# Optimization experiments

Hardware: AMD Instinct MI355X
Metric: run time of the kernel (lower is better)

The kernel has to match this reference:

```python
import jax, jax.numpy as jnp
import numpy as np

UP = 2      # up_ratio
K = 3       # kernel_size
EPS = 1e-5  # BatchNorm eps


def _bn(x, g, b, m, v):
    # eval-mode BatchNorm2d over channel axis 1 of NCHW
    scale = g / jnp.sqrt(v + EPS)
    return x * scale[:, None, None] + (b - m * scale)[:, None, None]


def setup_inputs() -> dict:
    key = jax.random.key(0)
    ks = jax.random.split(key, 13)
    N, C, H, W = 8, 256, 64, 64
    OC = 64
    P = UP * UP * K * K  # 36 encoder output channels
    return {
        "x": jax.random.normal(ks[0], (N, C, H, W), jnp.float32),
        "w0": jax.random.normal(ks[1], (OC, C), jnp.float32) * 0.05,
        "b0": jax.random.normal(ks[2], (OC,), jnp.float32) * 0.05,
        "bn0_g": jax.random.uniform(ks[3], (OC,), jnp.float32, 0.5, 1.5),
        "bn0_b": jax.random.normal(ks[4], (OC,), jnp.float32) * 0.05,
        "bn0_m": jax.random.normal(ks[5], (OC,), jnp.float32) * 0.05,
        "bn0_v": jax.random.uniform(ks[6], (OC,), jnp.float32, 0.5, 1.5),
        "w1": jax.random.normal(ks[7], (P, OC), jnp.float32) * 0.05,
        "b1": jax.random.normal(ks[8], (P,), jnp.float32) * 0.05,
        "bn1_g": jax.random.uniform(ks[9], (P,), jnp.float32, 0.5, 1.5),
        "bn1_b": jax.random.normal(ks[10], (P,), jnp.float32) * 0.05,
        "bn1_m": jax.random.normal(ks[11], (P,), jnp.float32) * 0.05,
        "bn1_v": jax.random.uniform(ks[12], (P,), jnp.float32, 0.5, 1.5),
    }


def reference(x, w0, b0, bn0_g, bn0_b, bn0_m, bn0_v,
              w1, b1, bn1_g, bn1_b, bn1_m, bn1_v):
    N, C, H, W = x.shape
    k2, u2 = K * K, UP * UP

    # layer0: 1x1 conv + BN + ReLU
    y = jnp.einsum('nchw,oc->nohw', x, w0) + b0[:, None, None]
    y = jax.nn.relu(_bn(y, bn0_g, bn0_b, bn0_m, bn0_v))

    # encoder: 1x1 conv + BN + ReLU -> (N, u2*k2, H, W)
    enc = jnp.einsum('nohw,po->nphw', y, w1) + b1[:, None, None]
    enc = jax.nn.relu(_bn(enc, bn1_g, bn1_b, bn1_m, bn1_v))

    # pixelshuffle(UP) + softmax over k2 + unfold back to low-res is
    # algebraically: split channels as (k2, u2) and softmax over k2.
    # channel index = k*u2 + r*UP + s, matching torch PixelShuffle layout.
    wts = jax.nn.softmax(enc.reshape(N, k2, u2, H, W), axis=1)  # n k u h w

    # im2col on input: ZeroPad2d(1) + 3x3 unfold -> (N, C, k2, H, W)
    pad = K // 2
    xp = jnp.pad(x, ((0, 0), (0, 0), (pad, pad), (pad, pad)))
    patches = jnp.stack([xp[:, :, i:i + H, j:j + W]
                         for i in range(K) for j in range(K)], axis=2)

    out = jnp.einsum('nckhw,nkuhw->ncuhw', patches, wts)  # (N, C, u2, H, W)

    # pixelshuffle: u = r*UP + s places value at (h*UP+r, w*UP+s)
    out = out.reshape(N, C, UP, UP, H, W)
    out = out.transpose(0, 1, 4, 2, 5, 3).reshape(N, C, H * UP, W * UP)
    return out
```

## Files before the change

kernel.cpp:

```cpp
#include <hip/hip_runtime.h>


#define EPS_BN 1e-5f

typedef float f32x4 __attribute__((ext_vector_type(4)));

__global__ __launch_bounds__(256) void carafe_fused(
    const float* __restrict__ x,
    const float* __restrict__ w0, const float* __restrict__ b0,
    const float* __restrict__ g0, const float* __restrict__ be0,
    const float* __restrict__ m0, const float* __restrict__ v0,
    const float* __restrict__ w1, const float* __restrict__ b1,
    const float* __restrict__ g1, const float* __restrict__ be1,
    const float* __restrict__ m1, const float* __restrict__ v1,
    float* __restrict__ out)
{
    __shared__ float xs[256 * 64];
    __shared__ float ys[64 * 64];

    const int tid = threadIdx.x;
    const int n   = blockIdx.x >> 6;
    const int hh  = blockIdx.x & 63;
    const int w   = tid & 63;
    const int og  = __builtin_amdgcn_readfirstlane(tid >> 6);

    {
        const f32x4* xg = reinterpret_cast<const f32x4*>(x + (n * 256) * 4096 + hh * 64);
        f32x4* xl = reinterpret_cast<f32x4*>(xs);
#pragma unroll
        for (int k = 0; k < 16; ++k) {
            const int i  = tid + k * 256;
            const int cc = i >> 4;
            const int c4 = i & 15;
            xl[cc * 16 + c4] = xg[cc * 1024 + c4];
        }
    }
    __syncthreads();

    float acc[16];
#pragma unroll
    for (int j = 0; j < 16; ++j) acc[j] = 0.f;

    const float* w0p = w0 + og * 16 * 256;
#pragma unroll 8
    for (int c = 0; c < 256; ++c) {
        const float xv = xs[c * 64 + w];
#pragma unroll
        for (int j = 0; j < 16; ++j)
            acc[j] = fmaf(xv, w0p[j * 256 + c], acc[j]);
    }

#pragma unroll
    for (int j = 0; j < 16; ++j) {
        const int o = og * 16 + j;
        const float sc = g0[o] * rsqrtf(v0[o] + EPS_BN);
        const float sh = (b0[o] - m0[o]) * sc + be0[o];
        ys[o * 64 + w] = fmaxf(fmaf(acc[j], sc, sh), 0.f);
    }
    __syncthreads();

    float e9[9];
#pragma unroll
    for (int kk = 0; kk < 9; ++kk) e9[kk] = 0.f;
    const int u = og;
    const float* w1p = w1 + u * 64;
#pragma unroll 4
    for (int o = 0; o < 64; ++o) {
        const float yv = ys[o * 64 + w];
#pragma unroll
        for (int kk = 0; kk < 9; ++kk)
            e9[kk] = fmaf(yv, w1p[kk * 256 + o], e9[kk]);
    }

    float mx = -1e30f;
#pragma unroll
    for (int kk = 0; kk < 9; ++kk) {
        const int p = kk * 4 + u;
        const float sc = g1[p] * rsqrtf(v1[p] + EPS_BN);
        const float sh = (b1[p] - m1[p]) * sc + be1[p];
        float e = fmaxf(fmaf(e9[kk], sc, sh), 0.f);
        e9[kk] = e;
        mx = fmaxf(mx, e);
    }
    float s = 0.f;
#pragma unroll
    for (int kk = 0; kk < 9; ++kk) {
        e9[kk] = __expf(e9[kk] - mx);
        s += e9[kk];
    }
    const float inv = 1.f / s;

    __syncthreads();
    float* ws = ys;
#pragma unroll
    for (int kk = 0; kk < 9; ++kk)
        ws[(kk * 4 + u) * 64 + w] = e9[kk] * inv;
    __syncthreads();

    const int q = og;
    float wt[36];
#pragma unroll
    for (int p = 0; p < 36; ++p) wt[p] = ws[p * 64 + w];

    const bool hm = (hh > 0), hp = (hh < 63);
    const bool wm = (w > 0),  wp = (w < 63);

    for (int c = 0; c < 64; ++c) {
        const int cc = q * 64 + c;
        const float* xgm = x + ((n * 256 + cc) * 64 + (hh - 1)) * 64;
        const float* xgp = x + ((n * 256 + cc) * 64 + (hh + 1)) * 64;
        const float* xls = xs + cc * 64;

        float a0 = 0.f, a1 = 0.f, a2 = 0.f, a3 = 0.f;

        {
            const float xv0 = (hm & wm) ? xgm[w - 1] : 0.f;
            const float xv1 = hm        ? xgm[w]     : 0.f;
            const float xv2 = (hm & wp) ? xgm[w + 1] : 0.f;
            a0 = fmaf(xv0, wt[0],  fmaf(xv1, wt[4],  xv2 * wt[8]));
            a1 = fmaf(xv0, wt[1],  fmaf(xv1, wt[5],  xv2 * wt[9]));
            a2 = fmaf(xv0, wt[2],  fmaf(xv1, wt[6],  xv2 * wt[10]));
            a3 = fmaf(xv0, wt[3],  fmaf(xv1, wt[7],  xv2 * wt[11]));
        }
        {
            const float xv0 = wm ? xls[w - 1] : 0.f;
            const float xv1 = xls[w];
            const float xv2 = wp ? xls[w + 1] : 0.f;
            a0 = fmaf(xv0, wt[12], fmaf(xv1, wt[16], fmaf(xv2, wt[20], a0)));
            a1 = fmaf(xv0, wt[13], fmaf(xv1, wt[17], fmaf(xv2, wt[21], a1)));
            a2 = fmaf(xv0, wt[14], fmaf(xv1, wt[18], fmaf(xv2, wt[22], a2)));
            a3 = fmaf(xv0, wt[15], fmaf(xv1, wt[19], fmaf(xv2, wt[23], a3)));
        }
        {
            const float xv0 = (hp & wm) ? xgp[w - 1] : 0.f;
            const float xv1 = hp        ? xgp[w]     : 0.f;
            const float xv2 = (hp & wp) ? xgp[w + 1] : 0.f;
            a0 = fmaf(xv0, wt[24], fmaf(xv1, wt[28], fmaf(xv2, wt[32], a0)));
            a1 = fmaf(xv0, wt[25], fmaf(xv1, wt[29], fmaf(xv2, wt[33], a1)));
            a2 = fmaf(xv0, wt[26], fmaf(xv1, wt[30], fmaf(xv2, wt[34], a2)));
            a3 = fmaf(xv0, wt[27], fmaf(xv1, wt[31], fmaf(xv2, wt[35], a3)));
        }

        float* op = out + ((n * 256 + cc) * 128 + 2 * hh) * 128 + 2 * w;
        float2 r0; r0.x = a0; r0.y = a1;
        float2 r1; r1.x = a2; r1.y = a3;
        *reinterpret_cast<float2*>(op)       = r0;
        *reinterpret_cast<float2*>(op + 128) = r1;
    }
}

extern "C" void kernel_launch(void* const* d_in, const int* in_sizes, int n_in,
                              void* d_out, int out_size, void* d_ws, size_t ws_size,
                              hipStream_t stream)
{
    const float* x   = (const float*)d_in[0];
    const float* w0  = (const float*)d_in[1];
    const float* b0  = (const float*)d_in[2];
    const float* g0  = (const float*)d_in[3];
    const float* be0 = (const float*)d_in[4];
    const float* m0  = (const float*)d_in[5];
    const float* v0  = (const float*)d_in[6];
    const float* w1  = (const float*)d_in[7];
    const float* b1  = (const float*)d_in[8];
    const float* g1  = (const float*)d_in[9];
    const float* be1 = (const float*)d_in[10];
    const float* m1  = (const float*)d_in[11];
    const float* v1  = (const float*)d_in[12];

    float* out = (float*)d_out;

    hipLaunchKernelGGL(carafe_fused, dim3(512), dim3(256), 0, stream,
                       x, w0, b0, g0, be0, m0, v0, w1, b1, g1, be1, m1, v1, out);
}
```

Baseline: 244.7 us.

## Drop 64KB input LDS stage and double block to 512 threads

```diff
diff --git a/kernel.cpp b/kernel.cpp
--- a/kernel.cpp
+++ b/kernel.cpp
@@ -3,9 +3,7 @@
 
 #define EPS_BN 1e-5f
 
-typedef float f32x4 __attribute__((ext_vector_type(4)));
-
-__global__ __launch_bounds__(256) void carafe_fused(
+__global__ __launch_bounds__(512, 4) void carafe_fused(
     const float* __restrict__ x,
     const float* __restrict__ w0, const float* __restrict__ b0,
     const float* __restrict__ g0, const float* __restrict__ be0,
@@ -15,7 +13,6 @@
     const float* __restrict__ m1, const float* __restrict__ v1,
     float* __restrict__ out)
 {
-    __shared__ float xs[256 * 64];
     __shared__ float ys[64 * 64];
 
     const int tid = threadIdx.x;
@@ -24,35 +21,24 @@
     const int w   = tid & 63;
     const int og  = __builtin_amdgcn_readfirstlane(tid >> 6);
 
-    {
-        const f32x4* xg = reinterpret_cast<const f32x4*>(x + (n * 256) * 4096 + hh * 64);
-        f32x4* xl = reinterpret_cast<f32x4*>(xs);
+    float acc[8];
 #pragma unroll
-        for (int k = 0; k < 16; ++k) {
-            const int i  = tid + k * 256;
-            const int cc = i >> 4;
-            const int c4 = i & 15;
-            xl[cc * 16 + c4] = xg[cc * 1024 + c4];
-        }
-    }
-    __syncthreads();
+    for (int j = 0; j < 8; ++j) acc[j] = 0.f;
 
-    float acc[16];
-#pragma unroll
-    for (int j = 0; j < 16; ++j) acc[j] = 0.f;
+    const float* xp  = x + n * 1048576 + hh * 64 + w;
+    const float* w0p = w0 + og * 8 * 256;
 
-    const float* w0p = w0 + og * 16 * 256;
 #pragma unroll 8
     for (int c = 0; c < 256; ++c) {
-        const float xv = xs[c * 64 + w];
+        const float xv = xp[c * 4096];
 #pragma unroll
-        for (int j = 0; j < 16; ++j)
+        for (int j = 0; j < 8; ++j)
             acc[j] = fmaf(xv, w0p[j * 256 + c], acc[j]);
     }
 
 #pragma unroll
-    for (int j = 0; j < 16; ++j) {
-        const int o = og * 16 + j;
+    for (int j = 0; j < 8; ++j) {
+        const int o = og * 8 + j;
         const float sc = g0[o] * rsqrtf(v0[o] + EPS_BN);
         const float sh = (b0[o] - m0[o]) * sc + be0[o];
         ys[o * 64 + w] = fmaxf(fmaf(acc[j], sc, sh), 0.f);
@@ -62,9 +48,9 @@
     float e9[9];
 #pragma unroll
     for (int kk = 0; kk < 9; ++kk) e9[kk] = 0.f;
-    const int u = og;
+    const int u = og & 3;
     const float* w1p = w1 + u * 64;
-#pragma unroll 4
+#pragma unroll 8
     for (int o = 0; o < 64; ++o) {
         const float yv = ys[o * 64 + w];
 #pragma unroll
@@ -91,50 +77,52 @@
     const float inv = 1.f / s;
 
     __syncthreads();
-    float* ws = ys;
+    if (og < 4) {
 #pragma unroll
-    for (int kk = 0; kk < 9; ++kk)
-        ws[(kk * 4 + u) * 64 + w] = e9[kk] * inv;
+        for (int kk = 0; kk < 9; ++kk)
+            ys[(kk * 4 + u) * 64 + w] = e9[kk] * inv;
+    }
     __syncthreads();
 
-    const int q = og;
     float wt[36];
 #pragma unroll
-    for (int p = 0; p < 36; ++p) wt[p] = ws[p * 64 + w];
+    for (int p = 0; p < 36; ++p) wt[p] = ys[p * 64 + w];
 
     const bool hm = (hh > 0), hp = (hh < 63);
     const bool wm = (w > 0),  wp = (w < 63);
+    const float* xrow = x + n * 1048576 + hh * 64;
 
-    for (int c = 0; c < 64; ++c) {
-        const int cc = q * 64 + c;
-        const float* xgm = x + ((n * 256 + cc) * 64 + (hh - 1)) * 64;
-        const float* xgp = x + ((n * 256 + cc) * 64 + (hh + 1)) * 64;
-        const float* xls = xs + cc * 64;
+#pragma unroll 2
+    for (int i = 0; i < 32; ++i) {
+        const int cc = og * 32 + i;
+        const float* xr = xrow + cc * 4096;
+        const float* xm = xr - 64;
+        const float* xq = xr + 64;
 
         float a0 = 0.f, a1 = 0.f, a2 = 0.f, a3 = 0.f;
 
         {
-            const float xv0 = (hm & wm) ? xgm[w - 1] : 0.f;
-            const float xv1 = hm        ? xgm[w]     : 0.f;
-            const float xv2 = (hm & wp) ? xgm[w + 1] : 0.f;
+            const float xv0 = (hm & wm) ? xm[w - 1] : 0.f;
+            const float xv1 = hm        ? xm[w]     : 0.f;
+            const float xv2 = (hm & wp) ? xm[w + 1] : 0.f;
             a0 = fmaf(xv0, wt[0],  fmaf(xv1, wt[4],  xv2 * wt[8]));
             a1 = fmaf(xv0, wt[1],  fmaf(xv1, wt[5],  xv2 * wt[9]));
             a2 = fmaf(xv0, wt[2],  fmaf(xv1, wt[6],  xv2 * wt[10]));
             a3 = fmaf(xv0, wt[3],  fmaf(xv1, wt[7],  xv2 * wt[11]));
         }
         {
-            const float xv0 = wm ? xls[w - 1] : 0.f;
-            const float xv1 = xls[w];
-            const float xv2 = wp ? xls[w + 1] : 0.f;
+            const float xv0 = wm ? xr[w - 1] : 0.f;
+            const float xv1 = xr[w];
+            const float xv2 = wp ? xr[w + 1] : 0.f;
             a0 = fmaf(xv0, wt[12], fmaf(xv1, wt[16], fmaf(xv2, wt[20], a0)));
             a1 = fmaf(xv0, wt[13], fmaf(xv1, wt[17], fmaf(xv2, wt[21], a1)));
             a2 = fmaf(xv0, wt[14], fmaf(xv1, wt[18], fmaf(xv2, wt[22], a2)));
             a3 = fmaf(xv0, wt[15], fmaf(xv1, wt[19], fmaf(xv2, wt[23], a3)));
         }
         {
-            const float xv0 = (hp & wm) ? xgp[w - 1] : 0.f;
-            const float xv1 = hp        ? xgp[w]     : 0.f;
-            const float xv2 = (hp & wp) ? xgp[w + 1] : 0.f;
+            const float xv0 = (hp & wm) ? xq[w - 1] : 0.f;
+            const float xv1 = hp        ? xq[w]     : 0.f;
+            const float xv2 = (hp & wp) ? xq[w + 1] : 0.f;
             a0 = fmaf(xv0, wt[24], fmaf(xv1, wt[28], fmaf(xv2, wt[32], a0)));
             a1 = fmaf(xv0, wt[25], fmaf(xv1, wt[29], fmaf(xv2, wt[33], a1)));
             a2 = fmaf(xv0, wt[26], fmaf(xv1, wt[30], fmaf(xv2, wt[34], a2)));
@@ -169,6 +157,6 @@
 
     float* out = (float*)d_out;
 
-    hipLaunchKernelGGL(carafe_fused, dim3(512), dim3(256), 0, stream,
+    hipLaunchKernelGGL(carafe_fused, dim3(512), dim3(512), 0, stream,
                        x, w0, b0, g0, be0, m0, v0, w1, b1, g1, be1, m1, v1, out);
 }
```

Measured after the change: 209.5 us. -14.4%, faster.
